# Kernel optimization log

Hardware: AMD Instinct MI355X
Metric: run time of the kernel (lower is better)

Reference implementation:

```python
import jax, jax.numpy as jnp
import numpy as np

IN_F = 2048
OUT_F = 2048
GRID = 5
BATCH = 16384

def setup_inputs() -> dict:
    key = jax.random.key(0)
    kx, kb, ks = jax.random.split(key, 3)
    x = jax.random.normal(kx, (BATCH, IN_F), dtype=jnp.float32)
    # kaiming_uniform_(a=sqrt(5)) on [out, in]: bound = sqrt(6/((1+5)*in)) = 1/sqrt(in)
    bound = 1.0 / np.sqrt(IN_F)
    base_weight = jax.random.uniform(kb, (OUT_F, IN_F), minval=-bound, maxval=bound, dtype=jnp.float32)
    spline_weights = jax.random.uniform(ks, (OUT_F, IN_F, GRID), minval=-0.1, maxval=0.1, dtype=jnp.float32)
    return {"x": x, "base_weight": base_weight, "spline_weights": spline_weights}

def reference(x, base_weight, spline_weights):
    # base path: SiLU then linear (no bias)
    base_out = jnp.einsum('bi,oi->bo', jax.nn.silu(x), base_weight)
    # RBF spline basis over fixed grid in [-1, 1]
    grid = jnp.linspace(-1.0, 1.0, GRID, dtype=x.dtype)  # [g]
    basis = jnp.exp(-((x[..., None] - grid) ** 2) * 5.0)  # [b, i, g]
    spline_out = jnp.einsum('big,oig->bo', basis, spline_weights)
    return base_out + spline_out
```

## Files before the change

### kernel.cpp

```cpp
#include <hip/hip_runtime.h>
#include <hip/hip_bf16.h>
#include <cstdint>
#include <cstddef>


#define KIN 2048
#define NOUT 2048
#define BATCH 16384
#define KEXP 12288
#define NKT 192

typedef __bf16 bf16x8 __attribute__((ext_vector_type(8)));
typedef float f32x4 __attribute__((ext_vector_type(4)));
typedef unsigned short u16x4 __attribute__((ext_vector_type(4)));

__device__ __forceinline__ unsigned short f2bf(float f) {
    union { float f; uint32_t u; } v; v.f = f;
    return (unsigned short)((v.u + 0x7FFFu + ((v.u >> 16) & 1u)) >> 16);
}

__device__ __forceinline__ void load_lds16(const void* gptr, void* lptr) {
    __builtin_amdgcn_global_load_lds(
        (const __attribute__((address_space(1))) unsigned int*)gptr,
        (__attribute__((address_space(3))) unsigned int*)lptr,
        16, 0, 0);
}

__global__ __launch_bounds__(256)
void expand_ab(const float* __restrict__ X, const float* __restrict__ BW,
               const float* __restrict__ SW, __bf16* __restrict__ Aexp,
               __bf16* __restrict__ Wexp)
{
    __shared__ __align__(16) __bf16 rowbuf[KEXP];
    const int bid = blockIdx.x;
    const int tid = threadIdx.x;

    if (bid >= NOUT) {
        const int row = bid - NOUT;
        const float* xrow = X + (size_t)row * KIN;
        const float K0 = 42.521082000062783f;
        const float K1 = 3.4903429574597902f;
        const float K2 = 0.2865047968601901f;
        const float K3 = 0.023517745856009107f;
        #pragma unroll
        for (int s = 0; s < 2; ++s) {
            const f32x4 xv = *(const f32x4*)(xrow + (s * 256 + tid) * 4);
            float o[24];
            #pragma unroll
            for (int e = 0; e < 4; ++e) {
                const float xf = xv[e];
                const float d0 = xf + 1.0f;
                float b = __expf(-5.0f * d0 * d0);
                const float s5 = __expf(5.0f * xf);
                o[e * 6 + 0] = b;
                b *= s5 * K0; o[e * 6 + 1] = b;
                b *= s5 * K1; o[e * 6 + 2] = b;
                b *= s5 * K2; o[e * 6 + 3] = b;
                b *= s5 * K3; o[e * 6 + 4] = b;
                o[e * 6 + 5] = xf / (1.0f + __expf(-xf));
            }
            __bf16* dst = rowbuf + (s * 1024 + tid * 4) * 6;
            #pragma unroll
            for (int q = 0; q < 3; ++q) {
                bf16x8 v;
                #pragma unroll
                for (int t = 0; t < 8; ++t) v[t] = (__bf16)o[q * 8 + t];
                *(bf16x8*)(dst + q * 8) = v;
            }
        }
        __syncthreads();
        bf16x8* out = (bf16x8*)(Aexp + (size_t)row * KEXP);
        const bf16x8* lsrc = (const bf16x8*)rowbuf;
        #pragma unroll
        for (int t = 0; t < 6; ++t)
            out[tid + t * 256] = lsrc[tid + t * 256];
    } else {
        const int orow = bid;
        #pragma unroll
        for (int s = 0; s < 2; ++s) {
            const int i0 = s * 1024 + tid * 4;
            const float* sb = SW + ((size_t)orow * KIN + i0) * 5;
            const f32x4 bw = *(const f32x4*)(BW + (size_t)orow * KIN + i0);
            float sw[20];
            #pragma unroll
            for (int q = 0; q < 5; ++q) {
                const f32x4 v = *(const f32x4*)(sb + q * 4);
                sw[q * 4 + 0] = v.x; sw[q * 4 + 1] = v.y;
                sw[q * 4 + 2] = v.z; sw[q * 4 + 3] = v.w;
            }
            __bf16* dst = rowbuf + (size_t)i0 * 6;
            #pragma unroll
            for (int q = 0; q < 3; ++q) {
                bf16x8 v;
                #pragma unroll
                for (int t = 0; t < 8; ++t) {
                    const int e = (q * 8 + t) / 6;
                    const int c = (q * 8 + t) % 6;
                    v[t] = (c < 5) ? (__bf16)sw[e * 5 + c] : (__bf16)bw[e];
                }
                *(bf16x8*)(dst + q * 8) = v;
            }
        }
        __syncthreads();
        bf16x8* out = (bf16x8*)(Wexp + (size_t)orow * KEXP);
        const bf16x8* lsrc = (const bf16x8*)rowbuf;
        #pragma unroll
        for (int t = 0; t < 6; ++t)
            out[tid + t * 256] = lsrc[tid + t * 256];
    }
}

__global__ __launch_bounds__(512, 2)
void gemm8(const __bf16* __restrict__ A, const __bf16* __restrict__ W,
           float* __restrict__ OUT)
{
    __shared__ __align__(16) __bf16 LDS[65536];
    __bf16* LA = LDS;
    __bf16* LB = LDS + 32768;

    const int tid  = threadIdx.x;
    const int lane = tid & 63;
    const int wave = tid >> 6;
    const int r    = lane & 15;
    const int quad = lane >> 4;
    const int wm   = wave >> 2;
    const int wn   = wave & 3;

    const int bid0 = blockIdx.x;
    const int bid  = (bid0 & 7) * 64 + (bid0 >> 3);
    const int mt  = bid >> 3;
    const int nt  = bid & 7;
    const int m0  = mt * 256;
    const int n0  = nt * 256;

    const int c0   = tid;
    const int c1   = tid + 512;
    const int row0 = c0 >> 2, row1 = c1 >> 2;
    const int j0   = (c0 & 3) ^ ((c0 >> 3) & 3);
    const int j1   = (c1 & 3) ^ ((c1 >> 3) & 3);
    const __bf16* srcA0 = A + (size_t)(m0 + row0) * KEXP + j0 * 8;
    const __bf16* srcA1 = A + (size_t)(m0 + row1) * KEXP + j1 * 8;
    const __bf16* srcB0 = W + (size_t)(n0 + row0) * KEXP + j0 * 8;
    const __bf16* srcB1 = W + (size_t)(n0 + row1) * KEXP + j1 * 8;

    const int dst0 = wave * 512;
    const int dst1 = 4096 + wave * 512;

    const int swz = (quad ^ ((r >> 1) & 3)) * 8;
    const __bf16* a_rd = LA + (wm * 128 + r) * 32 + swz;
    const __bf16* b_rd = LB + (wn * 64 + r) * 32 + swz;

    f32x4 acc[8][4];
    #pragma unroll
    for (int i = 0; i < 8; ++i)
        #pragma unroll
        for (int j = 0; j < 4; ++j)
            acc[i][j] = (f32x4){0.0f, 0.0f, 0.0f, 0.0f};

    bf16x8 af0[4], af1[4], bf[4];

#define BARX() asm volatile("s_barrier" ::: "memory")
#define VM6()  asm volatile("s_waitcnt vmcnt(6)" ::: "memory")

#define STAGE_A(buf, kh, kt) do { \
    const size_t ko = (size_t)(kt) * 64 + (kh) * 32; \
    load_lds16(srcA0 + ko, LA + ((buf) * 2 + (kh)) * 8192 + dst0); \
    load_lds16(srcA1 + ko, LA + ((buf) * 2 + (kh)) * 8192 + dst1); } while (0)

#define STAGE_B(buf, kh, kt) do { \
    const size_t ko = (size_t)(kt) * 64 + (kh) * 32; \
    load_lds16(srcB0 + ko, LB + ((buf) * 2 + (kh)) * 8192 + dst0); \
    load_lds16(srcB1 + ko, LB + ((buf) * 2 + (kh)) * 8192 + dst1); } while (0)

#define READ_AF(arr, buf, ks, a) do { \
    const __bf16* p_ = a_rd + ((buf) * 2 + (ks)) * 8192 + (a) * 2048; \
    arr[0] = *(const bf16x8*)(p_); \
    arr[1] = *(const bf16x8*)(p_ + 512); \
    arr[2] = *(const bf16x8*)(p_ + 1024); \
    arr[3] = *(const bf16x8*)(p_ + 1536); } while (0)

#define READ_B(buf, ks) do { \
    const __bf16* p_ = b_rd + ((buf) * 2 + (ks)) * 8192; \
    bf[0] = *(const bf16x8*)(p_); \
    bf[1] = *(const bf16x8*)(p_ + 512); \
    bf[2] = *(const bf16x8*)(p_ + 1024); \
    bf[3] = *(const bf16x8*)(p_ + 1536); } while (0)

#define MFMA16(frag, a) do { \
    __builtin_amdgcn_s_setprio(1); \
    _Pragma("unroll") \
    for (int mi_ = 0; mi_ < 4; ++mi_) { \
        _Pragma("unroll") \
        for (int nj_ = 0; nj_ < 4; ++nj_) \
            acc[(a) * 4 + mi_][nj_] = __builtin_amdgcn_mfma_f32_16x16x32_bf16( \
                frag[mi_], bf[nj_], acc[(a) * 4 + mi_][nj_], 0, 0, 0); \
    } \
    __builtin_amdgcn_s_setprio(0); } while (0)

    STAGE_B(0, 0, 0); STAGE_A(0, 0, 0); STAGE_B(0, 1, 0); STAGE_A(0, 1, 0);
    STAGE_B(1, 0, 1); STAGE_A(1, 0, 1); STAGE_B(1, 1, 1);
    VM6();
    BARX();

    for (int t = 0; t < 96; ++t) {
        const int kt1 = 2 * t + 1;
        const int sA  = (2 * t + 2 < NKT) ? 2 * t + 2 : NKT - 1;
        const int sB  = (2 * t + 3 < NKT) ? 2 * t + 3 : NKT - 1;

        READ_AF(af0, 0, 0, 0); READ_AF(af1, 0, 0, 1); READ_B(0, 0);
        STAGE_A(1, 1, kt1);
        BARX();
        MFMA16(af0, 0);
        STAGE_B(0, 0, sA);
        MFMA16(af1, 1);
        BARX();

        READ_AF(af1, 0, 1, 1); READ_AF(af0, 0, 1, 0); READ_B(0, 1);
        STAGE_A(0, 0, sA);
        BARX();
        MFMA16(af1, 1);
        STAGE_B(0, 1, sA);
        VM6();
        MFMA16(af0, 0);
        BARX();

        READ_AF(af0, 1, 0, 0); READ_AF(af1, 1, 0, 1); READ_B(1, 0);
        STAGE_A(0, 1, sA);
        BARX();
        MFMA16(af0, 0);
        STAGE_B(1, 0, sB);
        MFMA16(af1, 1);
        BARX();

        READ_AF(af1, 1, 1, 1); READ_AF(af0, 1, 1, 0); READ_B(1, 1);
        STAGE_A(1, 0, sB);
        BARX();
        MFMA16(af1, 1);
        STAGE_B(1, 1, sB);
        VM6();
        MFMA16(af0, 0);
        BARX();
    }

    #pragma unroll
    for (int fi = 0; fi < 8; ++fi) {
        #pragma unroll
        for (int nj = 0; nj < 4; ++nj) {
            const int col  = n0 + wn * 64 + nj * 16 + r;
            const int rowb = m0 + wm * 128 + fi * 16 + quad * 4;
            #pragma unroll
            for (int reg = 0; reg < 4; ++reg)
                OUT[(size_t)(rowb + reg) * NOUT + col] = acc[fi][nj][reg];
        }
    }
#undef BARX
#undef VM6
#undef STAGE_A
#undef STAGE_B
#undef READ_AF
#undef READ_B
#undef MFMA16
}

#define BM 128
#define BN 128
#define NF 16
#define BK 96
#define LDK 104

__global__ __launch_bounds__(256)
void kan_fused(const float* __restrict__ X, const float* __restrict__ BW,
               const float* __restrict__ SW, float* __restrict__ OUT)
{
    __shared__ __align__(16) unsigned short As[BM * LDK];
    __shared__ __align__(16) unsigned short Bs[BN * LDK];

    const int tid  = threadIdx.x;
    const int lane = tid & 63;
    const int wave = tid >> 6;
    const int mt = blockIdx.x >> 4;
    const int nt = blockIdx.x & 15;
    const int m0 = mt * BM;
    const int n0 = nt * BN;
    const int r    = lane & 15;
    const int quad = lane >> 4;
    const int wm = (wave & 1) * 64;
    const int wn = (wave >> 1) * 64;

    f32x4 acc[4][4];
    #pragma unroll
    for (int i = 0; i < 4; ++i)
        #pragma unroll
        for (int j = 0; j < 4; ++j)
            acc[i][j] = (f32x4){0.0f, 0.0f, 0.0f, 0.0f};

    for (int it = 0; it < KIN / NF; ++it) {
        const int i0 = it * NF;
        __syncthreads();
        #pragma unroll
        for (int s = 0; s < 2; ++s) {
            const int slot = tid + s * 256;
            const int row  = slot >> 2;
            const int fq   = slot & 3;
            const f32x4 xv = *(const f32x4*)(X + (size_t)(m0 + row) * KIN + i0 + fq * 4);
            unsigned short basv[20];
            unsigned short silv[4];
            #pragma unroll
            for (int e = 0; e < 4; ++e) {
                const float xf = xv[e];
                silv[e] = f2bf(xf / (1.0f + __expf(-xf)));
                #pragma unroll
                for (int c = 0; c < 5; ++c) {
                    const float d = xf - (-1.0f + 0.5f * (float)c);
                    basv[e * 5 + c] = f2bf(__expf(-5.0f * d * d));
                }
            }
            unsigned short* dst = As + row * LDK + fq * 20;
            #pragma unroll
            for (int q = 0; q < 5; ++q) {
                u16x4 v;
                v.x = basv[q * 4 + 0]; v.y = basv[q * 4 + 1];
                v.z = basv[q * 4 + 2]; v.w = basv[q * 4 + 3];
                *(u16x4*)(dst + q * 4) = v;
            }
            u16x4 sv;
            sv.x = silv[0]; sv.y = silv[1]; sv.z = silv[2]; sv.w = silv[3];
            *(u16x4*)(As + row * LDK + 80 + fq * 4) = sv;
        }
        {
            const int orow = tid >> 1;
            const int half = tid & 1;
            const float* sbase = SW + (size_t)(n0 + orow) * (KIN * 5) + i0 * 5 + half * 40;
            unsigned short* brow = Bs + orow * LDK + half * 40;
            #pragma unroll
            for (int p = 0; p < 10; ++p) {
                const f32x4 wv = *(const f32x4*)(sbase + p * 4);
                u16x4 v;
                v.x = f2bf(wv.x); v.y = f2bf(wv.y);
                v.z = f2bf(wv.z); v.w = f2bf(wv.w);
                *(u16x4*)(brow + p * 4) = v;
            }
        }
        #pragma unroll
        for (int s = 0; s < 2; ++s) {
            const int slot = tid + s * 256;
            const int row  = slot >> 2;
            const int fq   = slot & 3;
            const f32x4 wv = *(const f32x4*)(BW + (size_t)(n0 + row) * KIN + i0 + fq * 4);
            u16x4 v;
            v.x = f2bf(wv.x); v.y = f2bf(wv.y);
            v.z = f2bf(wv.z); v.w = f2bf(wv.w);
            *(u16x4*)(Bs + row * LDK + 80 + fq * 4) = v;
        }
        __syncthreads();
        #pragma unroll
        for (int ks = 0; ks < 3; ++ks) {
            bf16x8 af[4], bfr[4];
            #pragma unroll
            for (int mi = 0; mi < 4; ++mi)
                af[mi] = *(const bf16x8*)(As + (wm + mi * 16 + r) * LDK + ks * 32 + quad * 8);
            #pragma unroll
            for (int ni = 0; ni < 4; ++ni)
                bfr[ni] = *(const bf16x8*)(Bs + (wn + ni * 16 + r) * LDK + ks * 32 + quad * 8);
            #pragma unroll
            for (int mi = 0; mi < 4; ++mi)
                #pragma unroll
                for (int ni = 0; ni < 4; ++ni)
                    acc[mi][ni] = __builtin_amdgcn_mfma_f32_16x16x32_bf16(
                        af[mi], bfr[ni], acc[mi][ni], 0, 0, 0);
        }
    }
    #pragma unroll
    for (int mi = 0; mi < 4; ++mi) {
        #pragma unroll
        for (int ni = 0; ni < 4; ++ni) {
            const int col  = n0 + wn + ni * 16 + r;
            const int rowb = m0 + wm + mi * 16 + quad * 4;
            #pragma unroll
            for (int reg = 0; reg < 4; ++reg)
                OUT[(size_t)(rowb + reg) * NOUT + col] = acc[mi][ni][reg];
        }
    }
}

extern "C" void kernel_launch(void* const* d_in, const int* in_sizes, int n_in,
                              void* d_out, int out_size, void* d_ws, size_t ws_size,
                              hipStream_t stream) {
    const float* X  = (const float*)d_in[0];
    const float* BW = (const float*)d_in[1];
    const float* SW = (const float*)d_in[2];
    float* OUT = (float*)d_out;

    const size_t nA = (size_t)BATCH * KEXP;
    const size_t nW = (size_t)NOUT * KEXP;
    const size_t ws_need = (nA + nW) * sizeof(__bf16);

    if (ws_size >= ws_need) {
        __bf16* Aexp = (__bf16*)d_ws;
        __bf16* Wexp = Aexp + nA;
        expand_ab<<<dim3(NOUT + BATCH), dim3(256), 0, stream>>>(X, BW, SW, Aexp, Wexp);
        gemm8<<<dim3(512), dim3(512), 0, stream>>>(Aexp, Wexp, OUT);
    } else {
        kan_fused<<<dim3(128 * 16), dim3(256), 0, stream>>>(X, BW, SW, OUT);
    }
}
```

Baseline: 973.1 us.

## Software-pipeline LDS fragment reads with MFMA using double-buffered B fragments

Restructures the GEMM main loop so LDS reads of the next A/B fragments are issued right before or between MFMA groups, instead of all reads happening up front before each compute phase. Adds a second B-fragment register set and prefetches the first fragments before the loop and at the end of each iteration. The aim is to hide LDS read latency behind matrix-core work. In exchange it uses more VGPRs and relies on the existing barrier and vmcnt placement still ordering the earlier reads correctly.

```diff
diff --git a/kernel.cpp b/kernel.cpp
--- a/kernel.cpp
+++ b/kernel.cpp
@@ -157,7 +157,7 @@
         for (int j = 0; j < 4; ++j)
             acc[i][j] = (f32x4){0.0f, 0.0f, 0.0f, 0.0f};
 
-    bf16x8 af0[4], af1[4], bf[4];
+    bf16x8 afX[4], afY[4], bfA[4], bfB[4];
 
 #define BARX() asm volatile("s_barrier" ::: "memory")
 #define VM6()  asm volatile("s_waitcnt vmcnt(6)" ::: "memory")
@@ -172,28 +172,28 @@
     load_lds16(srcB0 + ko, LB + ((buf) * 2 + (kh)) * 8192 + dst0); \
     load_lds16(srcB1 + ko, LB + ((buf) * 2 + (kh)) * 8192 + dst1); } while (0)
 
-#define READ_AF(arr, buf, ks, a) do { \
+#define READ_A(arr, buf, ks, a) do { \
     const __bf16* p_ = a_rd + ((buf) * 2 + (ks)) * 8192 + (a) * 2048; \
     arr[0] = *(const bf16x8*)(p_); \
     arr[1] = *(const bf16x8*)(p_ + 512); \
     arr[2] = *(const bf16x8*)(p_ + 1024); \
     arr[3] = *(const bf16x8*)(p_ + 1536); } while (0)
 
-#define READ_B(buf, ks) do { \
+#define READ_BF(arr, buf, ks) do { \
     const __bf16* p_ = b_rd + ((buf) * 2 + (ks)) * 8192; \
-    bf[0] = *(const bf16x8*)(p_); \
-    bf[1] = *(const bf16x8*)(p_ + 512); \
-    bf[2] = *(const bf16x8*)(p_ + 1024); \
-    bf[3] = *(const bf16x8*)(p_ + 1536); } while (0)
-
-#define MFMA16(frag, a) do { \
+    arr[0] = *(const bf16x8*)(p_); \
+    arr[1] = *(const bf16x8*)(p_ + 512); \
+    arr[2] = *(const bf16x8*)(p_ + 1024); \
+    arr[3] = *(const bf16x8*)(p_ + 1536); } while (0)
+
+#define MFMA16(frag, bfr, a) do { \
     __builtin_amdgcn_s_setprio(1); \
     _Pragma("unroll") \
     for (int mi_ = 0; mi_ < 4; ++mi_) { \
         _Pragma("unroll") \
         for (int nj_ = 0; nj_ < 4; ++nj_) \
             acc[(a) * 4 + mi_][nj_] = __builtin_amdgcn_mfma_f32_16x16x32_bf16( \
-                frag[mi_], bf[nj_], acc[(a) * 4 + mi_][nj_], 0, 0, 0); \
+                frag[mi_], bfr[nj_], acc[(a) * 4 + mi_][nj_], 0, 0, 0); \
     } \
     __builtin_amdgcn_s_setprio(0); } while (0)
 
@@ -201,45 +201,56 @@
     STAGE_B(1, 0, 1); STAGE_A(1, 0, 1); STAGE_B(1, 1, 1);
     VM6();
     BARX();
+    READ_A(afX, 0, 0, 0);
+    READ_BF(bfA, 0, 0);
 
     for (int t = 0; t < 96; ++t) {
         const int kt1 = 2 * t + 1;
         const int sA  = (2 * t + 2 < NKT) ? 2 * t + 2 : NKT - 1;
         const int sB  = (2 * t + 3 < NKT) ? 2 * t + 3 : NKT - 1;
 
-        READ_AF(af0, 0, 0, 0); READ_AF(af1, 0, 0, 1); READ_B(0, 0);
         STAGE_A(1, 1, kt1);
         BARX();
-        MFMA16(af0, 0);
+        READ_A(afY, 0, 0, 1);
+        MFMA16(afX, bfA, 0);
         STAGE_B(0, 0, sA);
-        MFMA16(af1, 1);
-        BARX();
-
-        READ_AF(af1, 0, 1, 1); READ_AF(af0, 0, 1, 0); READ_B(0, 1);
+        READ_A(afX, 0, 1, 0);
+        READ_BF(bfB, 0, 1);
+        MFMA16(afY, bfA, 1);
+        BARX();
+
         STAGE_A(0, 0, sA);
         BARX();
-        MFMA16(af1, 1);
+        READ_A(afY, 0, 1, 1);
+        MFMA16(afX, bfB, 0);
         STAGE_B(0, 1, sA);
         VM6();
-        MFMA16(af0, 0);
-        BARX();
-
-        READ_AF(af0, 1, 0, 0); READ_AF(af1, 1, 0, 1); READ_B(1, 0);
+        MFMA16(afY, bfB, 1);
+        BARX();
+
         STAGE_A(0, 1, sA);
-        BARX();
-        MFMA16(af0, 0);
+        READ_A(afX, 1, 0, 0);
+        READ_BF(bfA, 1, 0);
+        BARX();
+        READ_A(afY, 1, 0, 1);
+        MFMA16(afX, bfA, 0);
         STAGE_B(1, 0, sB);
-        MFMA16(af1, 1);
-        BARX();
-
-        READ_AF(af1, 1, 1, 1); READ_AF(af0, 1, 1, 0); READ_B(1, 1);
+        READ_A(afX, 1, 1, 0);
+        READ_BF(bfB, 1, 1);
+        MFMA16(afY, bfA, 1);
+        BARX();
+
         STAGE_A(1, 0, sB);
         BARX();
-        MFMA16(af1, 1);
+        READ_A(afY, 1, 1, 1);
+        MFMA16(afX, bfB, 0);
         STAGE_B(1, 1, sB);
         VM6();
-        MFMA16(af0, 0);
-        BARX();
+        MFMA16(afY, bfB, 1);
+        BARX();
+
+        READ_A(afX, 0, 0, 0);
+        READ_BF(bfA, 0, 0);
     }
 
     #pragma unroll
@@ -257,8 +268,8 @@
 #undef VM6
 #undef STAGE_A
 #undef STAGE_B
-#undef READ_AF
-#undef READ_B
+#undef READ_A
+#undef READ_BF
 #undef MFMA16
 }
 
```

Result: no change. 963.6 us (-1.0%).
